# Kernel optimization log

Measured on AMD Instinct MI355X. Metric: run time of the kernel, lower is better.

The kernel has to match this reference:

```python
import jax, jax.numpy as jnp
import numpy as np

M, A, E, H = 2048, 64, 128, 256
NUM_BOND_TYPES, NUM_ATOM_TYPES = 4, 118

def setup_inputs() -> dict:
    key = jax.random.key(0)
    ks = jax.random.split(key, 12)
    s = 0.02
    return {
        'node_rep': jax.random.normal(ks[0], (M, A, H), jnp.float32),
        'edge_index': jax.random.randint(ks[1], (M, 2, E), 0, A, jnp.int32),
        'bond_type_target': jax.random.randint(ks[2], (M, E), 0, NUM_BOND_TYPES, jnp.int32),
        'atom_type_target': jax.random.randint(ks[3], (M, A), 0, NUM_ATOM_TYPES, jnp.int32),
        'Wp1': jax.random.normal(ks[4], (H, H), jnp.float32) * s, 'bp1': jnp.zeros((H,), jnp.float32),
        'Wp2': jax.random.normal(ks[5], (H, H), jnp.float32) * s, 'bp2': jnp.zeros((H,), jnp.float32),
        'Wb1': jax.random.normal(ks[6], (2 * H, H), jnp.float32) * s, 'bb1': jnp.zeros((H,), jnp.float32),
        'Wb2': jax.random.normal(ks[7], (H, NUM_BOND_TYPES), jnp.float32) * s, 'bb2': jnp.zeros((NUM_BOND_TYPES,), jnp.float32),
        'Wa1': jax.random.normal(ks[8], (H, H), jnp.float32) * s, 'ba1': jnp.zeros((H,), jnp.float32),
        'Wa2': jax.random.normal(ks[9], (H, NUM_ATOM_TYPES), jnp.float32) * s, 'ba2': jnp.zeros((NUM_ATOM_TYPES,), jnp.float32),
    }

def _mlp(x, W1, b1, W2, b2):
    return jnp.maximum(x @ W1 + b1, 0.0) @ W2 + b2

def reference(node_rep, edge_index, bond_type_target, atom_type_target,
              Wp1, bp1, Wp2, bp2, Wb1, bb1, Wb2, bb2, Wa1, ba1, Wa2, ba2):
    # bond_if_proj: per-atom 2-layer MLP (dropout=0 -> identity)  [M,A,H]
    proj = _mlp(node_rep, Wp1, bp1, Wp2, bp2)
    # gather bond endpoint reps: index_select over atoms per molecule  [M,E,H]
    start = jnp.take_along_axis(proj, edge_index[:, 0, :, None], axis=1)
    end = jnp.take_along_axis(proj, edge_index[:, 1, :, None], axis=1)
    bt_in = jnp.concatenate([start, end], axis=-1)            # [M,E,2H]
    bt_logits = _mlp(bt_in, Wb1, bb1, Wb2, bb2)               # [M,E,4]
    bt_logp = jax.nn.log_softmax(bt_logits, axis=-1)
    # per-molecule mean CE averaged over molecules == global mean (equal sizes)
    bond_type_loss = -jnp.mean(jnp.take_along_axis(bt_logp, bond_type_target[..., None], axis=-1))
    bond_type_acc = jnp.mean((jnp.argmax(bt_logits, axis=-1) == bond_type_target).astype(jnp.float32))
    # atom type classifier on raw node reps  [M,A,118]
    at_logits = _mlp(node_rep, Wa1, ba1, Wa2, ba2)
    at_logp = jax.nn.log_softmax(at_logits, axis=-1)
    atom_type_loss = -jnp.mean(jnp.take_along_axis(at_logp, atom_type_target[..., None], axis=-1))
    atom_type_acc = jnp.mean((jnp.argmax(at_logits, axis=-1) == atom_type_target).astype(jnp.float32))
    loss = 0.5 * bond_type_loss + 0.5 * atom_type_loss
    return loss, bond_type_acc, atom_type_acc
```

## Files before the change

kernel.cpp:

```cpp
#include <hip/hip_runtime.h>
#include <hip/hip_bf16.h>

typedef __bf16 bf16x8 __attribute__((ext_vector_type(8)));
typedef float f32x16 __attribute__((ext_vector_type(16)));

__device__ inline unsigned short f2bf(float f) {
  __hip_bfloat16 h = __float2bfloat16(f);
  return *reinterpret_cast<unsigned short*>(&h);
}
__device__ inline unsigned pack2bf(float a, float b) {
  return (unsigned)f2bf(a) | ((unsigned)f2bf(b) << 16);
}
__device__ inline uint2 pack4bf(float a, float b, float c, float d) {
  uint2 r; r.x = pack2bf(a, b); r.y = pack2bf(c, d); return r;
}
__device__ inline bf16x8 as_bf16x8(uint4 v) { return __builtin_bit_cast(bf16x8, v); }
__device__ inline float bitf(unsigned u) { return __builtin_bit_cast(float, u); }
__device__ inline f32x16 mfma16(bf16x8 a, bf16x8 b, f32x16 c) {
  return __builtin_amdgcn_mfma_f32_32x32x16_bf16(a, b, c, 0, 0, 0);
}

#define XADDR(kk) ((((xr) << 9) + ((kk) << 5) + (h << 4)) ^ xswz)

#define GEMM4(XB, WPTR, CBASE)                                                 \
  {                                                                            \
    const unsigned char* wb_ = (const unsigned char*)(WPTR) +                  \
                               (((CBASE) + l31) << 5) + (h << 4);              \
    acc0 = zero; acc1 = zero; acc2 = zero; acc3 = zero;                        \
    bf16x8 bva = *(const bf16x8*)((XB) + XADDR(0));                            \
    uint4 p0 = *(const uint4*)(wb_ + 0);                                       \
    uint4 p1 = *(const uint4*)(wb_ + 1024);                                    \
    uint4 p2 = *(const uint4*)(wb_ + 2048);                                    \
    uint4 p3 = *(const uint4*)(wb_ + 3072);                                    \
    _Pragma("unroll")                                                          \
    for (int kk = 0; kk < 16; kk += 2) {                                       \
      bf16x8 bvb = *(const bf16x8*)((XB) + XADDR(kk + 1));                     \
      uint4 q0 = *(const uint4*)(wb_ + ((kk + 1) << 13) + 0);                  \
      uint4 q1 = *(const uint4*)(wb_ + ((kk + 1) << 13) + 1024);               \
      uint4 q2 = *(const uint4*)(wb_ + ((kk + 1) << 13) + 2048);               \
      uint4 q3 = *(const uint4*)(wb_ + ((kk + 1) << 13) + 3072);               \
      acc0 = mfma16(as_bf16x8(p0), bva, acc0);                                 \
      acc1 = mfma16(as_bf16x8(p1), bva, acc1);                                 \
      acc2 = mfma16(as_bf16x8(p2), bva, acc2);                                 \
      acc3 = mfma16(as_bf16x8(p3), bva, acc3);                                 \
      if (kk + 2 < 16) {                                                       \
        bva = *(const bf16x8*)((XB) + XADDR(kk + 2));                          \
        p0 = *(const uint4*)(wb_ + ((kk + 2) << 13) + 0);                      \
        p1 = *(const uint4*)(wb_ + ((kk + 2) << 13) + 1024);                   \
        p2 = *(const uint4*)(wb_ + ((kk + 2) << 13) + 2048);                   \
        p3 = *(const uint4*)(wb_ + ((kk + 2) << 13) + 3072);                   \
      }                                                                        \
      acc0 = mfma16(as_bf16x8(q0), bvb, acc0);                                 \
      acc1 = mfma16(as_bf16x8(q1), bvb, acc1);                                 \
      acc2 = mfma16(as_bf16x8(q2), bvb, acc2);                                 \
      acc3 = mfma16(as_bf16x8(q3), bvb, acc3);                                 \
    }                                                                          \
  }

#define WB_TILE(DB, ACC, A, CBASE, BIASPTR, RELU)                              \
  _Pragma("unroll")                                                            \
  for (int g = 0; g < 4; ++g) {                                                \
    int col = (CBASE) + (A) * 32 + g * 8 + h * 4;                              \
    float4 bb = *(const float4*)((BIASPTR) + col);                             \
    float v0 = ACC[4 * g + 0] + bb.x;                                          \
    float v1 = ACC[4 * g + 1] + bb.y;                                          \
    float v2 = ACC[4 * g + 2] + bb.z;                                          \
    float v3 = ACC[4 * g + 3] + bb.w;                                          \
    if (RELU) { v0 = fmaxf(v0, 0.f); v1 = fmaxf(v1, 0.f);                      \
                v2 = fmaxf(v2, 0.f); v3 = fmaxf(v3, 0.f); }                    \
    int off = (((xr) << 9) + (col << 1)) ^ xswz;                               \
    *(uint2*)((DB) + off) = pack4bf(v0, v1, v2, v3);                           \
  }

#define WB_TILE_RAW(DB, ACC, A, CBASE)                                         \
  _Pragma("unroll")                                                            \
  for (int g = 0; g < 4; ++g) {                                                \
    int col = (CBASE) + (A) * 32 + g * 8 + h * 4;                              \
    int off = (((xr) << 9) + (col << 1)) ^ xswz;                               \
    *(uint2*)((DB) + off) = pack4bf(ACC[4 * g + 0], ACC[4 * g + 1],            \
                                    ACC[4 * g + 2], ACC[4 * g + 3]);           \
  }

__global__ __launch_bounds__(256) void k_pack(
    const float* __restrict__ wp1, const float* __restrict__ wa1,
    const float* __restrict__ wa2,
    unsigned short* __restrict__ dp1, unsigned short* __restrict__ da1,
    unsigned short* __restrict__ da2, float* __restrict__ accum)
{
  int b = blockIdx.x, tid = threadIdx.x;
  if (b == 0 && tid < 8) accum[tid] = 0.f;
  const float* src; unsigned short* dst; int e, logN, Nreal;
  if (b < 256)       { src = wp1; dst = dp1; e = b * 256 + tid;          logN = 8; Nreal = 256; }
  else if (b < 512)  { src = wa1; dst = da1; e = (b - 256) * 256 + tid;  logN = 8; Nreal = 256; }
  else               { src = wa2; dst = da2; e = (b - 512) * 256 + tid;  logN = 7; Nreal = 118; }
  int dk = e & 15;
  int rest = e >> 4;
  int n = rest & ((1 << logN) - 1);
  int kk = rest >> logN;
  int k = kk * 16 + dk;
  float v = (n < Nreal) ? src[k * Nreal + n] : 0.f;
  dst[e] = f2bf(v);
}

__global__ __launch_bounds__(256) void k_fold(
    const float* __restrict__ wp2, const float* __restrict__ wb1,
    const float* __restrict__ bp2, const float* __restrict__ bb1,
    unsigned short* __restrict__ dct, unsigned short* __restrict__ dcb,
    float* __restrict__ bias_e)
{
  int b = blockIdx.x, n = threadIdx.x;
  if (b < 512) {
    int k = b & 255;
    int off = (b < 256) ? 0 : 256;
    float s = 0.f;
    for (int t = 0; t < 256; ++t)
      s += wp2[k * 256 + t] * wb1[(t + off) * 256 + n];
    unsigned short* dst = (b < 256) ? dct : dcb;
    dst[((k >> 4) * 256 + n) * 16 + (k & 15)] = f2bf(s);
  } else {
    float s = bb1[n];
    for (int t = 0; t < 256; ++t)
      s += bp2[t] * (wb1[t * 256 + n] + wb1[(256 + t) * 256 + n]);
    bias_e[n] = s;
  }
}

__global__ __launch_bounds__(256, 2) void k_bond(
    const float* __restrict__ node, const int* __restrict__ eidx,
    const int* __restrict__ tgt,
    const unsigned short* __restrict__ wp1p, const float* __restrict__ bp1,
    const unsigned short* __restrict__ wctp, const unsigned short* __restrict__ wcbp,
    const float* __restrict__ bias_e, const float* __restrict__ wb2,
    const float* __restrict__ bb2, float* __restrict__ accum)
{
  __shared__ __align__(16) unsigned char bufA[32768];
  __shared__ __align__(16) unsigned char bufB[32768];
  __shared__ float s_bias[256];
  __shared__ float4 s_wb2[256];
  __shared__ float s_red[8];
  const int tid = threadIdx.x;
  const int lane = tid & 63;
  const int w = tid >> 6;
  const int l31 = lane & 31;
  const int h = lane >> 5;
  const int rb = w >> 1, cb = w & 1;
  const int m = blockIdx.x;

  {
    const float* src = node + (long)m * 16384;
    #pragma unroll
    for (int it = 0; it < 8; ++it) {
      int lb = (it * 256 + tid) * 16;
      int dst = lb ^ (((lb >> 9) & 7) << 4);
      const float4* s4 = (const float4*)(src + (lb >> 1));
      float4 f0 = s4[0], f1 = s4[1];
      uint4 v = { pack2bf(f0.x, f0.y), pack2bf(f0.z, f0.w),
                  pack2bf(f1.x, f1.y), pack2bf(f1.z, f1.w) };
      *(uint4*)(bufA + dst) = v;
    }
    s_bias[tid] = bias_e[tid];
    s_wb2[tid] = ((const float4*)wb2)[tid];
  }
  const int es = eidx[m * 256 + (tid >> 1)];
  const int ed = eidx[m * 256 + 128 + (tid >> 1)];
  const int etg = tgt[m * 128 + (tid >> 1)];
  const float q0 = bb2[0], q1 = bb2[1], q2 = bb2[2], q3 = bb2[3];
  __syncthreads();

  const int xr = rb * 32 + l31;
  const int xswz = (xr & 7) << 4;
  const int cbase = cb * 128;
  f32x16 zero = {};
  f32x16 acc0, acc1, acc2, acc3;

  GEMM4(bufA, wp1p, cbase);
  __syncthreads();
  WB_TILE(bufA, acc0, 0, cbase, bp1, 1);
  WB_TILE(bufA, acc1, 1, cbase, bp1, 1);
  WB_TILE(bufA, acc2, 2, cbase, bp1, 1);
  WB_TILE(bufA, acc3, 3, cbase, bp1, 1);
  __syncthreads();

  GEMM4(bufA, wctp, cbase);
  WB_TILE_RAW(bufB, acc0, 0, cbase);
  WB_TILE_RAW(bufB, acc1, 1, cbase);
  WB_TILE_RAW(bufB, acc2, 2, cbase);
  WB_TILE_RAW(bufB, acc3, 3, cbase);
  GEMM4(bufA, wcbp, cbase);
  __syncthreads();
  WB_TILE_RAW(bufA, acc0, 0, cbase);
  WB_TILE_RAW(bufA, acc1, 1, cbase);
  WB_TILE_RAW(bufA, acc2, 2, cbase);
  WB_TILE_RAW(bufA, acc3, 3, cbase);
  __syncthreads();

  {
    const int hf = tid & 1;
    float lg0 = 0.f, lg1 = 0.f, lg2 = 0.f, lg3 = 0.f;
    #pragma unroll
    for (int j = 0; j < 16; ++j) {
      int c0 = hf * 128 + j * 8;
      int offS = ((es << 9) + (c0 << 1)) ^ ((es & 7) << 4);
      int offD = ((ed << 9) + (c0 << 1)) ^ ((ed & 7) << 4);
      uint4 us = *(const uint4*)(bufB + offS);
      uint4 ud = *(const uint4*)(bufA + offD);
      const unsigned* pu = (const unsigned*)&us;
      const unsigned* pv = (const unsigned*)&ud;
      #pragma unroll
      for (int q = 0; q < 4; ++q) {
        unsigned ua = pu[q], ub = pv[q];
        int c = c0 + 2 * q;
        float hlo = bitf(ua << 16) + bitf(ub << 16) + s_bias[c];
        float hhi = bitf(ua & 0xffff0000u) + bitf(ub & 0xffff0000u) + s_bias[c + 1];
        hlo = fmaxf(hlo, 0.f); hhi = fmaxf(hhi, 0.f);
        float4 w0 = s_wb2[c], w1 = s_wb2[c + 1];
        lg0 = fmaf(hlo, w0.x, fmaf(hhi, w1.x, lg0));
        lg1 = fmaf(hlo, w0.y, fmaf(hhi, w1.y, lg1));
        lg2 = fmaf(hlo, w0.z, fmaf(hhi, w1.z, lg2));
        lg3 = fmaf(hlo, w0.w, fmaf(hhi, w1.w, lg3));
      }
    }
    lg0 += __shfl_xor(lg0, 1); lg1 += __shfl_xor(lg1, 1);
    lg2 += __shfl_xor(lg2, 1); lg3 += __shfl_xor(lg3, 1);
    float ce = 0.f, cc = 0.f;
    if (hf == 0) {
      float l0 = lg0 + q0, l1 = lg1 + q1, l2 = lg2 + q2, l3 = lg3 + q3;
      int t = etg;
      int am = 0; float mx = l0;
      if (l1 > mx) { mx = l1; am = 1; }
      if (l2 > mx) { mx = l2; am = 2; }
      if (l3 > mx) { mx = l3; am = 3; }
      float s = __expf(l0 - mx) + __expf(l1 - mx) + __expf(l2 - mx) + __expf(l3 - mx);
      float lt = (t == 0) ? l0 : (t == 1) ? l1 : (t == 2) ? l2 : l3;
      ce = __logf(s) + mx - lt;
      cc = (am == t) ? 1.f : 0.f;
    }
    #pragma unroll
    for (int d = 1; d < 64; d <<= 1) { ce += __shfl_xor(ce, d); cc += __shfl_xor(cc, d); }
    if (lane == 0) { s_red[w * 2] = ce; s_red[w * 2 + 1] = cc; }
    __syncthreads();
    if (tid == 0) {
      atomicAdd(accum + 0, s_red[0] + s_red[2] + s_red[4] + s_red[6]);
      atomicAdd(accum + 1, s_red[1] + s_red[3] + s_red[5] + s_red[7]);
    }
  }
}

__global__ __launch_bounds__(256, 2) void k_atom(
    const float* __restrict__ node,
    const unsigned short* __restrict__ w1p, const float* __restrict__ b1,
    const unsigned short* __restrict__ w2p, const float* __restrict__ b2,
    const int* __restrict__ tgt, float* __restrict__ accum)
{
  __shared__ __align__(16) unsigned char sm[65536];
  __shared__ float s_red[8];
  const int tid = threadIdx.x;
  const int lane = tid & 63;
  const int w = tid >> 6;
  const int l31 = lane & 31;
  const int h = lane >> 5;
  const long rowbase = (long)blockIdx.x * 128;

  {
    const float* src = node + rowbase * 256;
    #pragma unroll
    for (int it = 0; it < 16; ++it) {
      int lb = (it * 256 + tid) * 16;
      int dst = lb ^ (((lb >> 9) & 7) << 4);
      const float4* s4 = (const float4*)(src + (lb >> 1));
      float4 f0 = s4[0], f1 = s4[1];
      uint4 v = { pack2bf(f0.x, f0.y), pack2bf(f0.z, f0.w),
                  pack2bf(f1.x, f1.y), pack2bf(f1.z, f1.w) };
      *(uint4*)(sm + dst) = v;
    }
  }
  __syncthreads();

  const int xr = w * 32 + l31;
  const int xswz = (xr & 7) << 4;
  f32x16 zero = {};

  f32x16 c0 = zero, c1 = zero, c2 = zero, c3 = zero,
         c4 = zero, c5 = zero, c6 = zero, c7 = zero;
  {
    const unsigned char* wb_ = (const unsigned char*)w1p + (l31 << 5) + (h << 4);
    #pragma unroll
    for (int kk = 0; kk < 16; ++kk) {
      bf16x8 bv = *(const bf16x8*)(sm + XADDR(kk));
      const unsigned char* wk = wb_ + (kk << 13);
      uint4 r0 = *(const uint4*)(wk + 0);
      uint4 r1 = *(const uint4*)(wk + 1024);
      uint4 r2 = *(const uint4*)(wk + 2048);
      uint4 r3 = *(const uint4*)(wk + 3072);
      uint4 r4 = *(const uint4*)(wk + 4096);
      uint4 r5 = *(const uint4*)(wk + 5120);
      uint4 r6 = *(const uint4*)(wk + 6144);
      uint4 r7 = *(const uint4*)(wk + 7168);
      c0 = mfma16(as_bf16x8(r0), bv, c0);
      c1 = mfma16(as_bf16x8(r1), bv, c1);
      c2 = mfma16(as_bf16x8(r2), bv, c2);
      c3 = mfma16(as_bf16x8(r3), bv, c3);
      c4 = mfma16(as_bf16x8(r4), bv, c4);
      c5 = mfma16(as_bf16x8(r5), bv, c5);
      c6 = mfma16(as_bf16x8(r6), bv, c6);
      c7 = mfma16(as_bf16x8(r7), bv, c7);
    }
  }
  WB_TILE(sm, c0, 0, 0, b1, 1);
  WB_TILE(sm, c1, 1, 0, b1, 1);
  WB_TILE(sm, c2, 2, 0, b1, 1);
  WB_TILE(sm, c3, 3, 0, b1, 1);
  WB_TILE(sm, c4, 4, 0, b1, 1);
  WB_TILE(sm, c5, 5, 0, b1, 1);
  WB_TILE(sm, c6, 6, 0, b1, 1);
  WB_TILE(sm, c7, 7, 0, b1, 1);

  f32x16 e0 = zero, e1 = zero, e2 = zero, e3 = zero;
  {
    const unsigned char* wb_ = (const unsigned char*)w2p + (l31 << 5) + (h << 4);
    #pragma unroll
    for (int kk = 0; kk < 16; ++kk) {
      bf16x8 bv = *(const bf16x8*)(sm + XADDR(kk));
      const unsigned char* wk = wb_ + (kk << 12);
      e0 = mfma16(as_bf16x8(*(const uint4*)(wk + 0)), bv, e0);
      e1 = mfma16(as_bf16x8(*(const uint4*)(wk + 1024)), bv, e1);
      e2 = mfma16(as_bf16x8(*(const uint4*)(wk + 2048)), bv, e2);
      e3 = mfma16(as_bf16x8(*(const uint4*)(wk + 3072)), bv, e3);
    }
  }

  long grow = rowbase + xr;
  int t = tgt[grow];
  float mx = -3.0e38f; int am = 0;
  #define EPI_MAX(EV, AB)                                                      \
    _Pragma("unroll")                                                          \
    for (int q = 0; q < 16; ++q) {                                             \
      int col = (AB) + (q & 3) + 8 * (q >> 2) + 4 * h;                         \
      if (col < 118) {                                                         \
        float v = EV[q] + b2[col];                                             \
        EV[q] = v;                                                             \
        if (v > mx) { mx = v; am = col; }                                      \
      }                                                                        \
    }
  EPI_MAX(e0, 0) EPI_MAX(e1, 32) EPI_MAX(e2, 64) EPI_MAX(e3, 96)
  float omx = __shfl_xor(mx, 32); int oam = __shfl_xor(am, 32);
  if (omx > mx || (omx == mx && oam < am)) { mx = omx; am = oam; }
  float s = 0.f;
  #define EPI_SUM(EV, AB)                                                      \
    _Pragma("unroll")                                                          \
    for (int q = 0; q < 16; ++q) {                                             \
      int col = (AB) + (q & 3) + 8 * (q >> 2) + 4 * h;                         \
      if (col < 118) s += __expf(EV[q] - mx);                                  \
    }
  EPI_SUM(e0, 0) EPI_SUM(e1, 32) EPI_SUM(e2, 64) EPI_SUM(e3, 96)
  s += __shfl_xor(s, 32);
  float vt = 0.f;
  #define EPI_TGT(EV, AB)                                                      \
    _Pragma("unroll")                                                          \
    for (int q = 0; q < 16; ++q) {                                             \
      int col = (AB) + (q & 3) + 8 * (q >> 2) + 4 * h;                         \
      if (col < 118 && col == t) vt = EV[q];                                   \
    }
  EPI_TGT(e0, 0) EPI_TGT(e1, 32) EPI_TGT(e2, 64) EPI_TGT(e3, 96)
  vt += __shfl_xor(vt, 32);
  float ce = __logf(s) + mx - vt;
  float cc = (am == t) ? 1.f : 0.f;
  if (h) { ce = 0.f; cc = 0.f; }
  #pragma unroll
  for (int d = 1; d < 64; d <<= 1) { ce += __shfl_xor(ce, d); cc += __shfl_xor(cc, d); }
  if (lane == 0) { s_red[w * 2] = ce; s_red[w * 2 + 1] = cc; }
  __syncthreads();
  if (tid == 0) {
    atomicAdd(accum + 2, s_red[0] + s_red[2] + s_red[4] + s_red[6]);
    atomicAdd(accum + 3, s_red[1] + s_red[3] + s_red[5] + s_red[7]);
  }
}

__global__ __launch_bounds__(64) void k_final(const float* __restrict__ accum,
                                              float* __restrict__ out)
{
  if (threadIdx.x == 0) {
    float bce = accum[0] / 262144.f;
    float bcc = accum[1] / 262144.f;
    float ace = accum[2] / 131072.f;
    float acc_ = accum[3] / 131072.f;
    out[0] = 0.5f * bce + 0.5f * ace;
    out[1] = bcc;
    out[2] = acc_;
  }
}

extern "C" void kernel_launch(void* const* d_in, const int* in_sizes, int n_in,
                              void* d_out, int out_size, void* d_ws, size_t ws_size,
                              hipStream_t stream)
{
  const float* node = (const float*)d_in[0];
  const int* eidx   = (const int*)d_in[1];
  const int* btt    = (const int*)d_in[2];
  const int* att    = (const int*)d_in[3];
  const float* Wp1 = (const float*)d_in[4];
  const float* bp1 = (const float*)d_in[5];
  const float* Wp2 = (const float*)d_in[6];
  const float* bp2 = (const float*)d_in[7];
  const float* Wb1 = (const float*)d_in[8];
  const float* bb1 = (const float*)d_in[9];
  const float* Wb2 = (const float*)d_in[10];
  const float* bb2 = (const float*)d_in[11];
  const float* Wa1 = (const float*)d_in[12];
  const float* ba1 = (const float*)d_in[13];
  const float* Wa2 = (const float*)d_in[14];
  const float* ba2 = (const float*)d_in[15];

  char* ws = (char*)d_ws;
  float* accum = (float*)ws;
  unsigned short* dp1 = (unsigned short*)(ws + 256);
  unsigned short* da1 = (unsigned short*)(ws + 131328);
  unsigned short* da2 = (unsigned short*)(ws + 262400);
  unsigned short* dct = (unsigned short*)(ws + 327936);
  unsigned short* dcb = (unsigned short*)(ws + 459008);
  float* bias_e       = (float*)(ws + 590080);

  k_pack<<<640, 256, 0, stream>>>(Wp1, Wa1, Wa2, dp1, da1, da2, accum);
  k_fold<<<513, 256, 0, stream>>>(Wp2, Wb1, bp2, bb1, dct, dcb, bias_e);
  k_atom<<<1024, 256, 0, stream>>>(node, da1, ba1, da2, ba2, att, accum);
  k_bond<<<2048, 256, 0, stream>>>(node, eidx, btt, dp1, bp1, dct, dcb,
                                   bias_e, Wb2, bb2, accum);
  k_final<<<1, 64, 0, stream>>>(accum, (float*)d_out);
}
```

Before: 235.4 us.

## Retile bond and atom GEMMs to 2x2 warp tiles, halve atom block rows

Both kernels switch from per-warp 32-row x 128-column tiles to 64-row x 64-column warp tiles (2x2 MFMA blocks). Each A and B fragment load is now shared by two MFMAs, which cuts per-MFMA global weight loads. The atom kernel now processes 64 rows per block with a smaller shared buffer and 4 blocks/SM launch bounds, doubling the grid. Its softmax/CE epilogue now stages logits through shared memory and runs on 128 threads instead of using register-resident shuffles. The risk is extra shared traffic and syncs in the atom epilogue, and idle threads there.

```diff
diff --git a/kernel.cpp b/kernel.cpp
--- a/kernel.cpp
+++ b/kernel.cpp
@@ -20,65 +20,75 @@
   return __builtin_amdgcn_mfma_f32_32x32x16_bf16(a, b, c, 0, 0, 0);
 }
 
-#define XADDR(kk) ((((xr) << 9) + ((kk) << 5) + (h << 4)) ^ xswz)
-
-#define GEMM4(XB, WPTR, CBASE)                                                 \
+#define BADDR(XB, R, KK)                                                       \
+  ((XB) + (((((R) * 32 + l31) << 9) + ((KK) << 5) + (h << 4)) ^ swz))
+
+#define GEMM22(XB, WPTR, CW_)                                                  \
   {                                                                            \
     const unsigned char* wb_ = (const unsigned char*)(WPTR) +                  \
-                               (((CBASE) + l31) << 5) + (h << 4);              \
-    acc0 = zero; acc1 = zero; acc2 = zero; acc3 = zero;                        \
-    bf16x8 bva = *(const bf16x8*)((XB) + XADDR(0));                            \
-    uint4 p0 = *(const uint4*)(wb_ + 0);                                       \
-    uint4 p1 = *(const uint4*)(wb_ + 1024);                                    \
-    uint4 p2 = *(const uint4*)(wb_ + 2048);                                    \
-    uint4 p3 = *(const uint4*)(wb_ + 3072);                                    \
+                               (((CW_) + l31) << 5) + (h << 4);                \
+    acc00 = zero; acc01 = zero; acc10 = zero; acc11 = zero;                    \
+    bf16x8 pB0 = *(const bf16x8*)BADDR(XB, 0, 0);                              \
+    bf16x8 pB1 = *(const bf16x8*)BADDR(XB, 1, 0);                              \
+    uint4 pA0 = *(const uint4*)(wb_ + 0);                                      \
+    uint4 pA1 = *(const uint4*)(wb_ + 1024);                                   \
     _Pragma("unroll")                                                          \
     for (int kk = 0; kk < 16; kk += 2) {                                       \
-      bf16x8 bvb = *(const bf16x8*)((XB) + XADDR(kk + 1));                     \
-      uint4 q0 = *(const uint4*)(wb_ + ((kk + 1) << 13) + 0);                  \
-      uint4 q1 = *(const uint4*)(wb_ + ((kk + 1) << 13) + 1024);               \
-      uint4 q2 = *(const uint4*)(wb_ + ((kk + 1) << 13) + 2048);               \
-      uint4 q3 = *(const uint4*)(wb_ + ((kk + 1) << 13) + 3072);               \
-      acc0 = mfma16(as_bf16x8(p0), bva, acc0);                                 \
-      acc1 = mfma16(as_bf16x8(p1), bva, acc1);                                 \
-      acc2 = mfma16(as_bf16x8(p2), bva, acc2);                                 \
-      acc3 = mfma16(as_bf16x8(p3), bva, acc3);                                 \
+      bf16x8 qB0 = *(const bf16x8*)BADDR(XB, 0, kk + 1);                       \
+      bf16x8 qB1 = *(const bf16x8*)BADDR(XB, 1, kk + 1);                       \
+      uint4 qA0 = *(const uint4*)(wb_ + ((kk + 1) << 13));                     \
+      uint4 qA1 = *(const uint4*)(wb_ + ((kk + 1) << 13) + 1024);              \
+      acc00 = mfma16(as_bf16x8(pA0), pB0, acc00);                              \
+      acc10 = mfma16(as_bf16x8(pA1), pB0, acc10);                              \
+      acc01 = mfma16(as_bf16x8(pA0), pB1, acc01);                              \
+      acc11 = mfma16(as_bf16x8(pA1), pB1, acc11);                              \
       if (kk + 2 < 16) {                                                       \
-        bva = *(const bf16x8*)((XB) + XADDR(kk + 2));                          \
-        p0 = *(const uint4*)(wb_ + ((kk + 2) << 13) + 0);                      \
-        p1 = *(const uint4*)(wb_ + ((kk + 2) << 13) + 1024);                   \
-        p2 = *(const uint4*)(wb_ + ((kk + 2) << 13) + 2048);                   \
-        p3 = *(const uint4*)(wb_ + ((kk + 2) << 13) + 3072);                   \
+        pB0 = *(const bf16x8*)BADDR(XB, 0, kk + 2);                            \
+        pB1 = *(const bf16x8*)BADDR(XB, 1, kk + 2);                            \
+        pA0 = *(const uint4*)(wb_ + ((kk + 2) << 13));                         \
+        pA1 = *(const uint4*)(wb_ + ((kk + 2) << 13) + 1024);                  \
       }                                                                        \
-      acc0 = mfma16(as_bf16x8(q0), bvb, acc0);                                 \
-      acc1 = mfma16(as_bf16x8(q1), bvb, acc1);                                 \
-      acc2 = mfma16(as_bf16x8(q2), bvb, acc2);                                 \
-      acc3 = mfma16(as_bf16x8(q3), bvb, acc3);                                 \
+      acc00 = mfma16(as_bf16x8(qA0), qB0, acc00);                              \
+      acc10 = mfma16(as_bf16x8(qA1), qB0, acc10);                              \
+      acc01 = mfma16(as_bf16x8(qA0), qB1, acc01);                              \
+      acc11 = mfma16(as_bf16x8(qA1), qB1, acc11);                              \
     }                                                                          \
   }
 
-#define WB_TILE(DB, ACC, A, CBASE, BIASPTR, RELU)                              \
+#define WB22(DB, ACC, R, C, CW_, BIASPTR)                                      \
   _Pragma("unroll")                                                            \
   for (int g = 0; g < 4; ++g) {                                                \
-    int col = (CBASE) + (A) * 32 + g * 8 + h * 4;                              \
+    int xr_ = (R) * 32 + l31;                                                  \
+    int col = (CW_) + (C) * 32 + g * 8 + h * 4;                                \
     float4 bb = *(const float4*)((BIASPTR) + col);                             \
-    float v0 = ACC[4 * g + 0] + bb.x;                                          \
-    float v1 = ACC[4 * g + 1] + bb.y;                                          \
-    float v2 = ACC[4 * g + 2] + bb.z;                                          \
-    float v3 = ACC[4 * g + 3] + bb.w;                                          \
-    if (RELU) { v0 = fmaxf(v0, 0.f); v1 = fmaxf(v1, 0.f);                      \
-                v2 = fmaxf(v2, 0.f); v3 = fmaxf(v3, 0.f); }                    \
-    int off = (((xr) << 9) + (col << 1)) ^ xswz;                               \
+    float v0 = fmaxf(ACC[4 * g + 0] + bb.x, 0.f);                              \
+    float v1 = fmaxf(ACC[4 * g + 1] + bb.y, 0.f);                              \
+    float v2 = fmaxf(ACC[4 * g + 2] + bb.z, 0.f);                              \
+    float v3 = fmaxf(ACC[4 * g + 3] + bb.w, 0.f);                              \
+    int off = ((xr_ << 9) + (col << 1)) ^ ((xr_ & 7) << 4);                    \
     *(uint2*)((DB) + off) = pack4bf(v0, v1, v2, v3);                           \
   }
 
-#define WB_TILE_RAW(DB, ACC, A, CBASE)                                         \
+#define WB22R(DB, ACC, R, C, CW_)                                              \
   _Pragma("unroll")                                                            \
   for (int g = 0; g < 4; ++g) {                                                \
-    int col = (CBASE) + (A) * 32 + g * 8 + h * 4;                              \
-    int off = (((xr) << 9) + (col << 1)) ^ xswz;                               \
+    int xr_ = (R) * 32 + l31;                                                  \
+    int col = (CW_) + (C) * 32 + g * 8 + h * 4;                                \
+    int off = ((xr_ << 9) + (col << 1)) ^ ((xr_ & 7) << 4);                    \
     *(uint2*)((DB) + off) = pack4bf(ACC[4 * g + 0], ACC[4 * g + 1],            \
                                     ACC[4 * g + 2], ACC[4 * g + 3]);           \
+  }
+
+#define STAGE_X(DST, SRC)                                                      \
+  _Pragma("unroll")                                                            \
+  for (int it = 0; it < 8; ++it) {                                             \
+    int lb = (it * 256 + tid) * 16;                                            \
+    int d_ = lb ^ (((lb >> 9) & 7) << 4);                                      \
+    const float4* s4 = (const float4*)((SRC) + (lb >> 1));                     \
+    float4 f0 = s4[0], f1 = s4[1];                                             \
+    uint4 v_ = { pack2bf(f0.x, f0.y), pack2bf(f0.z, f0.w),                     \
+                 pack2bf(f1.x, f1.y), pack2bf(f1.z, f1.w) };                   \
+    *(uint4*)((DST) + d_) = v_;                                                \
   }
 
 __global__ __launch_bounds__(256) void k_pack(
@@ -143,55 +153,41 @@
   const int w = tid >> 6;
   const int l31 = lane & 31;
   const int h = lane >> 5;
-  const int rb = w >> 1, cb = w & 1;
+  const int swz = (l31 & 7) << 4;
+  const int CW = w * 64;
   const int m = blockIdx.x;
 
-  {
-    const float* src = node + (long)m * 16384;
-    #pragma unroll
-    for (int it = 0; it < 8; ++it) {
-      int lb = (it * 256 + tid) * 16;
-      int dst = lb ^ (((lb >> 9) & 7) << 4);
-      const float4* s4 = (const float4*)(src + (lb >> 1));
-      float4 f0 = s4[0], f1 = s4[1];
-      uint4 v = { pack2bf(f0.x, f0.y), pack2bf(f0.z, f0.w),
-                  pack2bf(f1.x, f1.y), pack2bf(f1.z, f1.w) };
-      *(uint4*)(bufA + dst) = v;
-    }
-    s_bias[tid] = bias_e[tid];
-    s_wb2[tid] = ((const float4*)wb2)[tid];
-  }
+  STAGE_X(bufA, node + (long)m * 16384);
+  s_bias[tid] = bias_e[tid];
+  s_wb2[tid] = ((const float4*)wb2)[tid];
+  __syncthreads();
+
+  f32x16 zero = {};
+  f32x16 acc00, acc01, acc10, acc11;
+
+  GEMM22(bufA, wp1p, CW);
+  __syncthreads();
+  WB22(bufA, acc00, 0, 0, CW, bp1);
+  WB22(bufA, acc10, 0, 1, CW, bp1);
+  WB22(bufA, acc01, 1, 0, CW, bp1);
+  WB22(bufA, acc11, 1, 1, CW, bp1);
+  __syncthreads();
+
+  GEMM22(bufA, wctp, CW);
+  WB22R(bufB, acc00, 0, 0, CW);
+  WB22R(bufB, acc10, 0, 1, CW);
+  WB22R(bufB, acc01, 1, 0, CW);
+  WB22R(bufB, acc11, 1, 1, CW);
+  GEMM22(bufA, wcbp, CW);
   const int es = eidx[m * 256 + (tid >> 1)];
   const int ed = eidx[m * 256 + 128 + (tid >> 1)];
   const int etg = tgt[m * 128 + (tid >> 1)];
-  const float q0 = bb2[0], q1 = bb2[1], q2 = bb2[2], q3 = bb2[3];
-  __syncthreads();
-
-  const int xr = rb * 32 + l31;
-  const int xswz = (xr & 7) << 4;
-  const int cbase = cb * 128;
-  f32x16 zero = {};
-  f32x16 acc0, acc1, acc2, acc3;
-
-  GEMM4(bufA, wp1p, cbase);
-  __syncthreads();
-  WB_TILE(bufA, acc0, 0, cbase, bp1, 1);
-  WB_TILE(bufA, acc1, 1, cbase, bp1, 1);
-  WB_TILE(bufA, acc2, 2, cbase, bp1, 1);
-  WB_TILE(bufA, acc3, 3, cbase, bp1, 1);
-  __syncthreads();
-
-  GEMM4(bufA, wctp, cbase);
-  WB_TILE_RAW(bufB, acc0, 0, cbase);
-  WB_TILE_RAW(bufB, acc1, 1, cbase);
-  WB_TILE_RAW(bufB, acc2, 2, cbase);
-  WB_TILE_RAW(bufB, acc3, 3, cbase);
-  GEMM4(bufA, wcbp, cbase);
-  __syncthreads();
-  WB_TILE_RAW(bufA, acc0, 0, cbase);
-  WB_TILE_RAW(bufA, acc1, 1, cbase);
-  WB_TILE_RAW(bufA, acc2, 2, cbase);
-  WB_TILE_RAW(bufA, acc3, 3, cbase);
+  const float b20 = bb2[0], b21 = bb2[1], b22 = bb2[2], b23 = bb2[3];
+  __syncthreads();
+  WB22R(bufA, acc00, 0, 0, CW);
+  WB22R(bufA, acc10, 0, 1, CW);
+  WB22R(bufA, acc01, 1, 0, CW);
+  WB22R(bufA, acc11, 1, 1, CW);
   __syncthreads();
 
   {
@@ -224,7 +220,7 @@
     lg2 += __shfl_xor(lg2, 1); lg3 += __shfl_xor(lg3, 1);
     float ce = 0.f, cc = 0.f;
     if (hf == 0) {
-      float l0 = lg0 + q0, l1 = lg1 + q1, l2 = lg2 + q2, l3 = lg3 + q3;
+      float l0 = lg0 + b20, l1 = lg1 + b21, l2 = lg2 + b22, l3 = lg3 + b23;
       int t = etg;
       int am = 0; float mx = l0;
       if (l1 > mx) { mx = l1; am = 1; }
@@ -246,126 +242,105 @@
   }
 }
 
-__global__ __launch_bounds__(256, 2) void k_atom(
+__global__ __launch_bounds__(256, 4) void k_atom(
     const float* __restrict__ node,
     const unsigned short* __restrict__ w1p, const float* __restrict__ b1,
     const unsigned short* __restrict__ w2p, const float* __restrict__ b2,
     const int* __restrict__ tgt, float* __restrict__ accum)
 {
-  __shared__ __align__(16) unsigned char sm[65536];
+  __shared__ __align__(16) unsigned char sm[33280];
   __shared__ float s_red[8];
   const int tid = threadIdx.x;
   const int lane = tid & 63;
   const int w = tid >> 6;
   const int l31 = lane & 31;
   const int h = lane >> 5;
-  const long rowbase = (long)blockIdx.x * 128;
-
+  const int swz = (l31 & 7) << 4;
+  const int CW = w * 64;
+  const long rowbase = (long)blockIdx.x * 64;
+
+  STAGE_X(sm, node + rowbase * 256);
+  __syncthreads();
+
+  f32x16 zero = {};
+  f32x16 acc00, acc01, acc10, acc11;
+
+  GEMM22(sm, w1p, CW);
+  __syncthreads();
+  WB22(sm, acc00, 0, 0, CW, b1);
+  WB22(sm, acc10, 0, 1, CW, b1);
+  WB22(sm, acc01, 1, 0, CW, b1);
+  WB22(sm, acc11, 1, 1, CW, b1);
+  __syncthreads();
+
+  f32x16 accL0 = zero, accL1 = zero;
   {
-    const float* src = node + rowbase * 256;
+    const int cw2 = w * 32;
+    const unsigned char* wb_ = (const unsigned char*)w2p +
+                               ((cw2 + l31) << 5) + (h << 4);
+    bf16x8 pB0 = *(const bf16x8*)BADDR(sm, 0, 0);
+    bf16x8 pB1 = *(const bf16x8*)BADDR(sm, 1, 0);
+    uint4 pA = *(const uint4*)(wb_);
     #pragma unroll
-    for (int it = 0; it < 16; ++it) {
-      int lb = (it * 256 + tid) * 16;
-      int dst = lb ^ (((lb >> 9) & 7) << 4);
-      const float4* s4 = (const float4*)(src + (lb >> 1));
-      float4 f0 = s4[0], f1 = s4[1];
-      uint4 v = { pack2bf(f0.x, f0.y), pack2bf(f0.z, f0.w),
-                  pack2bf(f1.x, f1.y), pack2bf(f1.z, f1.w) };
-      *(uint4*)(sm + dst) = v;
-    }
-  }
-  __syncthreads();
-
-  const int xr = w * 32 + l31;
-  const int xswz = (xr & 7) << 4;
-  f32x16 zero = {};
-
-  f32x16 c0 = zero, c1 = zero, c2 = zero, c3 = zero,
-         c4 = zero, c5 = zero, c6 = zero, c7 = zero;
+    for (int kk = 0; kk < 16; kk += 2) {
+      bf16x8 qB0 = *(const bf16x8*)BADDR(sm, 0, kk + 1);
+      bf16x8 qB1 = *(const bf16x8*)BADDR(sm, 1, kk + 1);
+      uint4 qA = *(const uint4*)(wb_ + ((kk + 1) << 12));
+      accL0 = mfma16(as_bf16x8(pA), pB0, accL0);
+      accL1 = mfma16(as_bf16x8(pA), pB1, accL1);
+      if (kk + 2 < 16) {
+        pB0 = *(const bf16x8*)BADDR(sm, 0, kk + 2);
+        pB1 = *(const bf16x8*)BADDR(sm, 1, kk + 2);
+        pA = *(const uint4*)(wb_ + ((kk + 2) << 12));
+      }
+      accL0 = mfma16(as_bf16x8(qA), qB0, accL0);
+      accL1 = mfma16(as_bf16x8(qA), qB1, accL1);
+    }
+  }
+  __syncthreads();
+
   {
-    const unsigned char* wb_ = (const unsigned char*)w1p + (l31 << 5) + (h << 4);
+    float* lgf = (float*)sm;
+    const int cw2 = w * 32;
     #pragma unroll
-    for (int kk = 0; kk < 16; ++kk) {
-      bf16x8 bv = *(const bf16x8*)(sm + XADDR(kk));
-      const unsigned char* wk = wb_ + (kk << 13);
-      uint4 r0 = *(const uint4*)(wk + 0);
-      uint4 r1 = *(const uint4*)(wk + 1024);
-      uint4 r2 = *(const uint4*)(wk + 2048);
-      uint4 r3 = *(const uint4*)(wk + 3072);
-      uint4 r4 = *(const uint4*)(wk + 4096);
-      uint4 r5 = *(const uint4*)(wk + 5120);
-      uint4 r6 = *(const uint4*)(wk + 6144);
-      uint4 r7 = *(const uint4*)(wk + 7168);
-      c0 = mfma16(as_bf16x8(r0), bv, c0);
-      c1 = mfma16(as_bf16x8(r1), bv, c1);
-      c2 = mfma16(as_bf16x8(r2), bv, c2);
-      c3 = mfma16(as_bf16x8(r3), bv, c3);
-      c4 = mfma16(as_bf16x8(r4), bv, c4);
-      c5 = mfma16(as_bf16x8(r5), bv, c5);
-      c6 = mfma16(as_bf16x8(r6), bv, c6);
-      c7 = mfma16(as_bf16x8(r7), bv, c7);
-    }
-  }
-  WB_TILE(sm, c0, 0, 0, b1, 1);
-  WB_TILE(sm, c1, 1, 0, b1, 1);
-  WB_TILE(sm, c2, 2, 0, b1, 1);
-  WB_TILE(sm, c3, 3, 0, b1, 1);
-  WB_TILE(sm, c4, 4, 0, b1, 1);
-  WB_TILE(sm, c5, 5, 0, b1, 1);
-  WB_TILE(sm, c6, 6, 0, b1, 1);
-  WB_TILE(sm, c7, 7, 0, b1, 1);
-
-  f32x16 e0 = zero, e1 = zero, e2 = zero, e3 = zero;
-  {
-    const unsigned char* wb_ = (const unsigned char*)w2p + (l31 << 5) + (h << 4);
-    #pragma unroll
-    for (int kk = 0; kk < 16; ++kk) {
-      bf16x8 bv = *(const bf16x8*)(sm + XADDR(kk));
-      const unsigned char* wk = wb_ + (kk << 12);
-      e0 = mfma16(as_bf16x8(*(const uint4*)(wk + 0)), bv, e0);
-      e1 = mfma16(as_bf16x8(*(const uint4*)(wk + 1024)), bv, e1);
-      e2 = mfma16(as_bf16x8(*(const uint4*)(wk + 2048)), bv, e2);
-      e3 = mfma16(as_bf16x8(*(const uint4*)(wk + 3072)), bv, e3);
-    }
-  }
-
-  long grow = rowbase + xr;
-  int t = tgt[grow];
-  float mx = -3.0e38f; int am = 0;
-  #define EPI_MAX(EV, AB)                                                      \
-    _Pragma("unroll")                                                          \
-    for (int q = 0; q < 16; ++q) {                                             \
-      int col = (AB) + (q & 3) + 8 * (q >> 2) + 4 * h;                         \
-      if (col < 118) {                                                         \
-        float v = EV[q] + b2[col];                                             \
-        EV[q] = v;                                                             \
-        if (v > mx) { mx = v; am = col; }                                      \
-      }                                                                        \
-    }
-  EPI_MAX(e0, 0) EPI_MAX(e1, 32) EPI_MAX(e2, 64) EPI_MAX(e3, 96)
-  float omx = __shfl_xor(mx, 32); int oam = __shfl_xor(am, 32);
-  if (omx > mx || (omx == mx && oam < am)) { mx = omx; am = oam; }
-  float s = 0.f;
-  #define EPI_SUM(EV, AB)                                                      \
-    _Pragma("unroll")                                                          \
-    for (int q = 0; q < 16; ++q) {                                             \
-      int col = (AB) + (q & 3) + 8 * (q >> 2) + 4 * h;                         \
-      if (col < 118) s += __expf(EV[q] - mx);                                  \
-    }
-  EPI_SUM(e0, 0) EPI_SUM(e1, 32) EPI_SUM(e2, 64) EPI_SUM(e3, 96)
-  s += __shfl_xor(s, 32);
-  float vt = 0.f;
-  #define EPI_TGT(EV, AB)                                                      \
-    _Pragma("unroll")                                                          \
-    for (int q = 0; q < 16; ++q) {                                             \
-      int col = (AB) + (q & 3) + 8 * (q >> 2) + 4 * h;                         \
-      if (col < 118 && col == t) vt = EV[q];                                   \
-    }
-  EPI_TGT(e0, 0) EPI_TGT(e1, 32) EPI_TGT(e2, 64) EPI_TGT(e3, 96)
-  vt += __shfl_xor(vt, 32);
-  float ce = __logf(s) + mx - vt;
-  float cc = (am == t) ? 1.f : 0.f;
-  if (h) { ce = 0.f; cc = 0.f; }
+    for (int q = 0; q < 16; ++q) {
+      int col = cw2 + (q & 3) + 8 * (q >> 2) + 4 * h;
+      if (col < 118) {
+        float bv = b2[col];
+        lgf[(l31) * 130 + col] = accL0[q] + bv;
+        lgf[(32 + l31) * 130 + col] = accL1[q] + bv;
+      }
+    }
+  }
+  __syncthreads();
+
+  float ce = 0.f, cc = 0.f;
+  if (tid < 128) {
+    const float* lgf = (const float*)sm;
+    int row = tid >> 1, h2 = tid & 1;
+    int t = tgt[rowbase + row];
+    const float* lr = lgf + row * 130;
+    int c0 = h2 * 59;
+    float mx = -3.0e38f; int am = 127;
+    for (int j = 0; j < 59; ++j) {
+      float v = lr[c0 + j];
+      if (v > mx) { mx = v; am = c0 + j; }
+    }
+    float mo = __shfl_xor(mx, 1); int amo = __shfl_xor(am, 1);
+    if (mo > mx || (mo == mx && amo < am)) { mx = mo; am = amo; }
+    float s = 0.f, vt = 0.f;
+    for (int j = 0; j < 59; ++j) {
+      float v = lr[c0 + j];
+      s += __expf(v - mx);
+      if (c0 + j == t) vt = v;
+    }
+    s += __shfl_xor(s, 1);
+    vt += __shfl_xor(vt, 1);
+    if (h2 == 0) {
+      ce = __logf(s) + mx - vt;
+      cc = (am == t) ? 1.f : 0.f;
+    }
+  }
   #pragma unroll
   for (int d = 1; d < 64; d <<= 1) { ce += __shfl_xor(ce, d); cc += __shfl_xor(cc, d); }
   if (lane == 0) { s_red[w * 2] = ce; s_red[w * 2 + 1] = cc; }
@@ -422,7 +397,7 @@
 
   k_pack<<<640, 256, 0, stream>>>(Wp1, Wa1, Wa2, dp1, da1, da2, accum);
   k_fold<<<513, 256, 0, stream>>>(Wp2, Wb1, bp2, bb1, dct, dcb, bias_e);
-  k_atom<<<1024, 256, 0, stream>>>(node, da1, ba1, da2, ba2, att, accum);
+  k_atom<<<2048, 256, 0, stream>>>(node, da1, ba1, da2, ba2, att, accum);
   k_bond<<<2048, 256, 0, stream>>>(node, eidx, btt, dp1, bp1, dct, dcb,
                                    bias_e, Wb2, bb2, accum);
   k_final<<<1, 64, 0, stream>>>(accum, (float*)d_out);
```

Measured after the change: 246.2 us. 4.6% more time.
